# Kernel tuning notes

Measured on AMD Instinct MI355X. Metric: run time of the kernel, lower is better.

The kernel has to match this reference:

```python
import jax, jax.numpy as jnp
import numpy as np

B, E, H = 4096, 8, 1024
XDIM, ZDIM, ODIM, GH = 800, 64, 768, 128

def setup_inputs() -> dict:
    key = jax.random.key(0)
    ks = jax.random.split(key, 16)
    s = lambda k, shape, fan: jax.random.normal(k, shape, jnp.float32) / np.sqrt(fan)
    return {
        'x': jax.random.normal(ks[0], (B, XDIM), jnp.float32),
        'z': jax.random.normal(ks[1], (B, ZDIM), jnp.float32),
        'Wg1': s(ks[2], (GH, XDIM + ZDIM), XDIM + ZDIM),
        'bg1': jnp.zeros((GH,), jnp.float32),
        'Wg2': s(ks[3], (GH, GH), GH),
        'bg2': jnp.zeros((GH,), jnp.float32),
        'Wg3': s(ks[4], (E, GH), GH),
        'bg3': jnp.zeros((E,), jnp.float32),
        'W0': s(ks[5], (E, H, XDIM + ZDIM), XDIM + ZDIM),
        'b0': jnp.zeros((E, H), jnp.float32),
        'W1': s(ks[6], (E, H, H + ZDIM), H + ZDIM),
        'b1': jnp.zeros((E, H), jnp.float32),
        'W2': s(ks[7], (E, H, H + ZDIM), H + ZDIM),
        'b2': jnp.zeros((E, H), jnp.float32),
        'W3': s(ks[8], (E, ODIM, H), H),
        'b3': jnp.zeros((E, ODIM), jnp.float32),
    }

def _blended_layer(bc, inp, W, b):
    # equivalent to (sum_e bc_e W_e) @ inp + sum_e bc_e b_e, but computed as
    # per-expert matmul then weighted accumulation (avoids [B,out,in] blend).
    y = jnp.einsum('bi,eoi->beo', inp, W)          # per-expert outputs
    return jnp.einsum('be,beo->bo', bc, y) + bc @ b

def reference(x, z, Wg1, bg1, Wg2, bg2, Wg3, bg3,
              W0, b0, W1, b1, W2, b2, W3, b3):
    g = jnp.concatenate([x, z], axis=1)
    h = jax.nn.elu(g @ Wg1.T + bg1)
    h = jax.nn.elu(h @ Wg2.T + bg2)
    bc = jax.nn.softmax(h @ Wg3.T + bg3, axis=-1)  # [B, E] blend coefficients
    h = jax.nn.elu(_blended_layer(bc, jnp.concatenate([x, z], 1), W0, b0))
    h = jax.nn.elu(_blended_layer(bc, jnp.concatenate([h, z], 1), W1, b1))
    h = jax.nn.elu(_blended_layer(bc, jnp.concatenate([h, z], 1), W2, b2))
    return _blended_layer(bc, h, W3, b3)  # [B, ODIM], no activation
```

## Files before the change

kernel.cpp:

```cpp
#include <hip/hip_runtime.h>
#include <math.h>

#define BDIM 4096
#define NEXP 8
#define HDIM 1024
#define XDIM 800
#define ZDIM 64
#define ODIM 768
#define GH   128

typedef _Float16 f16;
typedef f16   f16x8 __attribute__((ext_vector_type(8)));
typedef f16   f16x4 __attribute__((ext_vector_type(4)));
typedef float f32x4 __attribute__((ext_vector_type(4)));

__device__ __forceinline__ float elu_act(float x) {
    return x > 0.0f ? x : expm1f(x);
}

__device__ __forceinline__ void glds16(const void* g, void* l) {
    __builtin_amdgcn_global_load_lds(
        (const __attribute__((address_space(1))) void*)g,
        (__attribute__((address_space(3))) void*)l, 16, 0, 0);
}

__device__ __forceinline__ f16x8 vscale(f16x8 v, f16 s) {
    f16x8 r;
    #pragma unroll
    for (int i = 0; i < 8; ++i) r[i] = v[i] * s;
    return r;
}

#define BMg 64
#define BNg 64
#define BKg 32
#define PADg 68

template<int ACT>
__global__ __launch_bounds__(256)
void gemm_cat(const float* __restrict__ srcA, int KH,
              const float* __restrict__ srcZ, int KZ,
              const float* __restrict__ W, const float* __restrict__ bias,
              float* __restrict__ dst, int N)
{
    __shared__ float lds_a[BKg][PADg];
    __shared__ float lds_b[BKg][PADg];
    const int K = KH + KZ;
    const int row0 = blockIdx.x * BMg;
    const int col0 = blockIdx.y * BNg;
    const int tid = threadIdx.x;
    const int tx = tid & 15, ty = tid >> 4;

    float acc[4][4] = {};

    for (int k0 = 0; k0 < K; k0 += BKg) {
        #pragma unroll
        for (int it = 0; it < 2; ++it) {
            int idx = tid + it * 256;
            int r = idx >> 3;
            int f = idx & 7;
            int k = k0 + f * 4;
            const float* src; int col;
            if (k < KH) { src = srcA + (size_t)(row0 + r) * KH; col = k; }
            else        { src = srcZ + (size_t)(row0 + r) * KZ; col = k - KH; }
            float4 v = *(const float4*)(src + col);
            lds_a[f*4+0][r] = v.x; lds_a[f*4+1][r] = v.y;
            lds_a[f*4+2][r] = v.z; lds_a[f*4+3][r] = v.w;
        }
        #pragma unroll
        for (int it = 0; it < 2; ++it) {
            int idx = tid + it * 256;
            int c = idx >> 3;
            int f = idx & 7;
            int k = k0 + f * 4;
            float4 v = *(const float4*)(W + (size_t)(col0 + c) * K + k);
            lds_b[f*4+0][c] = v.x; lds_b[f*4+1][c] = v.y;
            lds_b[f*4+2][c] = v.z; lds_b[f*4+3][c] = v.w;
        }
        __syncthreads();
        #pragma unroll
        for (int j = 0; j < BKg; ++j) {
            float4 a4 = *(const float4*)&lds_a[j][ty*4];
            float4 b4 = *(const float4*)&lds_b[j][tx*4];
            float a[4] = {a4.x, a4.y, a4.z, a4.w};
            float b[4] = {b4.x, b4.y, b4.z, b4.w};
            #pragma unroll
            for (int i = 0; i < 4; ++i)
                #pragma unroll
                for (int jj = 0; jj < 4; ++jj)
                    acc[i][jj] += a[i] * b[jj];
        }
        __syncthreads();
    }

    #pragma unroll
    for (int i = 0; i < 4; ++i) {
        int r = row0 + ty*4 + i;
        float vals[4];
        #pragma unroll
        for (int j = 0; j < 4; ++j) {
            float v = acc[i][j] + bias[col0 + tx*4 + j];
            vals[j] = (ACT == 1) ? elu_act(v) : v;
        }
        *(float4*)(dst + (size_t)r * N + col0 + tx*4) =
            make_float4(vals[0], vals[1], vals[2], vals[3]);
    }
}

__global__ __launch_bounds__(256)
void gating3_softmax(const float* __restrict__ g2, const float* __restrict__ Wg3,
                     const float* __restrict__ bg3, float* __restrict__ bc)
{
    __shared__ float w[NEXP * GH];
    __shared__ float bsh[NEXP];
    const int tid = threadIdx.x;
    for (int i = tid; i < NEXP * GH; i += 256) w[i] = Wg3[i];
    if (tid < NEXP) bsh[tid] = bg3[tid];
    __syncthreads();

    const int rowl = tid >> 3;
    const int o    = tid & 7;
    const int row  = blockIdx.x * 32 + rowl;
    const float* g = g2 + (size_t)row * GH;

    float s = bsh[o];
    for (int k = 0; k < GH; ++k) s += g[k] * w[o * GH + k];

    float m = s;
    #pragma unroll
    for (int d = 4; d >= 1; d >>= 1) m = fmaxf(m, __shfl_xor(m, d, 8));
    float e = expf(s - m);
    float sum = e;
    #pragma unroll
    for (int d = 4; d >= 1; d >>= 1) sum += __shfl_xor(sum, d, 8);

    bc[(size_t)blockIdx.x * 256 + tid] = e / sum;
}

__global__ __launch_bounds__(256)
void fill_z(const float* __restrict__ z, f16* __restrict__ hz_a,
            f16* __restrict__ hz_b)
{
    int i = (blockIdx.x * 256 + threadIdx.x) * 4;
    int row = i >> 6;
    int col = i & 63;
    float4 v = *(const float4*)(z + i);
    f16x4 o = { (f16)v.x, (f16)v.y, (f16)v.z, (f16)v.w };
    size_t off = (size_t)row * (HDIM + ZDIM) + HDIM + col;
    *(f16x4*)(hz_a + off) = o;
    *(f16x4*)(hz_b + off) = o;
}

__global__ __launch_bounds__(256)
void w_to_f16(const float* __restrict__ src, f16* __restrict__ dst)
{
    size_t i = ((size_t)blockIdx.x * 256 + threadIdx.x) * 8;
    float4 v0 = *(const float4*)(src + i);
    float4 v1 = *(const float4*)(src + i + 4);
    f16x8 o = { (f16)v0.x,(f16)v0.y,(f16)v0.z,(f16)v0.w,
                (f16)v1.x,(f16)v1.y,(f16)v1.z,(f16)v1.w };
    *(f16x8*)(dst + i) = o;
}

template<int KE, int N, int ACT, int SRC, typename OT>
__global__ __launch_bounds__(256, 2)
void blended_big(const f16* __restrict__ A, int ldA,
                 const float* __restrict__ x, const float* __restrict__ z,
                 const f16* __restrict__ Wf, const float* __restrict__ bias,
                 const float* __restrict__ bc, OT* __restrict__ out, int ldOut)
{
    constexpr int NCT = N / 128;
    __shared__ __align__(16) f16 a_sh[64][40];
    __shared__ __align__(16) f16 b_sh[NEXP * 128 * 32];
    __shared__ float bc_sh[64][8];
    __shared__ float bias_sh[8][128];

    const int tid  = threadIdx.x;
    const int bid  = blockIdx.x;
    const int row0 = (bid / NCT) * 64;
    const int col0 = (bid % NCT) * 128;
    const int wave = tid >> 6;
    const int lane = tid & 63;
    const int ln   = lane & 15;
    const int quad = lane >> 4;
    const int wy   = wave >> 1;
    const int wx   = wave & 1;

    for (int i = tid; i < 64 * 8; i += 256)
        bc_sh[i >> 3][i & 7] = bc[(size_t)(row0 + (i >> 3)) * NEXP + (i & 7)];
    for (int i = tid; i < 8 * 128; i += 256)
        bias_sh[i >> 7][i & 127] = bias[(size_t)(i >> 7) * N + col0 + (i & 127)];

    f16 bcf[2][8];
    #pragma unroll
    for (int mi = 0; mi < 2; ++mi) {
        const float* bp = bc + (size_t)(row0 + wy*32 + mi*16 + ln) * NEXP;
        #pragma unroll
        for (int e = 0; e < NEXP; ++e) bcf[mi][e] = (f16)bp[e];
    }

    const int ar = tid >> 2;
    const int ac = tid & 3;
    const int kcl  = (lane & 3) ^ ((lane >> 3) & 3);
    const int prow = lane >> 2;
    const f16* wb[2];
    #pragma unroll
    for (int ee = 0; ee < 2; ++ee)
        wb[ee] = Wf + ((size_t)(wave*2 + ee) * N + col0 + prow) * KE + kcl * 8;

    const int csel = quad ^ ((ln >> 1) & 3);

    f32x4 acc[2][4] = {};

    for (int k0 = 0; k0 < KE; k0 += 32) {
        __syncthreads();

        #pragma unroll
        for (int ee = 0; ee < 2; ++ee) {
            const int e = wave * 2 + ee;
            #pragma unroll
            for (int j = 0; j < 8; ++j) {
                glds16(wb[ee] + k0 + (size_t)j * 16 * KE,
                       &b_sh[(e * 128 + j * 16) * 32]);
            }
        }

        f16x8 av;
        if (SRC == 0) {
            int k = k0 + ac * 8;
            const float* s = (k < XDIM)
                ? x + (size_t)(row0 + ar) * XDIM + k
                : z + (size_t)(row0 + ar) * ZDIM + (k - XDIM);
            float4 v0 = *(const float4*)s;
            float4 v1 = *(const float4*)(s + 4);
            av = (f16x8){ (f16)v0.x,(f16)v0.y,(f16)v0.z,(f16)v0.w,
                          (f16)v1.x,(f16)v1.y,(f16)v1.z,(f16)v1.w };
        } else {
            av = *(const f16x8*)(A + (size_t)(row0 + ar) * ldA + k0 + ac * 8);
        }
        *(f16x8*)&a_sh[ar][ac * 8] = av;

        __syncthreads();

        f16x8 af0 = *(const f16x8*)&a_sh[wy*32 +      ln][quad * 8];
        f16x8 af1 = *(const f16x8*)&a_sh[wy*32 + 16 + ln][quad * 8];

        #pragma unroll
        for (int e = 0; e < NEXP; ++e) {
            f16x8 bf[4];
            #pragma unroll
            for (int ni = 0; ni < 4; ++ni) {
                int n = wx*64 + ni*16 + ln;
                bf[ni] = *(const f16x8*)&b_sh[e*4096 + n*32 + csel*8];
            }
            f16x8 a0 = vscale(af0, bcf[0][e]);
            f16x8 a1 = vscale(af1, bcf[1][e]);
            #pragma unroll
            for (int ni = 0; ni < 4; ++ni) {
                acc[0][ni] = __builtin_amdgcn_mfma_f32_16x16x32_f16(
                    a0, bf[ni], acc[0][ni], 0, 0, 0);
                acc[1][ni] = __builtin_amdgcn_mfma_f32_16x16x32_f16(
                    a1, bf[ni], acc[1][ni], 0, 0, 0);
            }
        }
    }

    #pragma unroll
    for (int mi = 0; mi < 2; ++mi)
        #pragma unroll
        for (int r = 0; r < 4; ++r) {
            int rl = wy*32 + mi*16 + quad*4 + r;
            size_t grow = (size_t)(row0 + rl) * ldOut;
            #pragma unroll
            for (int ni = 0; ni < 4; ++ni) {
                int cl = wx*64 + ni*16 + ln;
                float v = acc[mi][ni][r];
                #pragma unroll
                for (int e2 = 0; e2 < NEXP; ++e2)
                    v += bc_sh[rl][e2] * bias_sh[e2][cl];
                if (ACT) v = elu_act(v);
                out[grow + col0 + cl] = (OT)v;
            }
        }
}

extern "C" void kernel_launch(void* const* d_in, const int* in_sizes, int n_in,
                              void* d_out, int out_size, void* d_ws, size_t ws_size,
                              hipStream_t stream)
{
    const float* x   = (const float*)d_in[0];
    const float* z   = (const float*)d_in[1];
    const float* Wg1 = (const float*)d_in[2];
    const float* bg1 = (const float*)d_in[3];
    const float* Wg2 = (const float*)d_in[4];
    const float* bg2 = (const float*)d_in[5];
    const float* Wg3 = (const float*)d_in[6];
    const float* bg3 = (const float*)d_in[7];
    const float* W0  = (const float*)d_in[8];
    const float* b0  = (const float*)d_in[9];
    const float* W1  = (const float*)d_in[10];
    const float* b1  = (const float*)d_in[11];
    const float* W2  = (const float*)d_in[12];
    const float* b2  = (const float*)d_in[13];
    const float* W3  = (const float*)d_in[14];
    const float* b3  = (const float*)d_in[15];
    float* out = (float*)d_out;

    char* ws = (char*)d_ws;
    f16*   wbuf = (f16*)ws;                 ws += (size_t)NEXP * HDIM * (HDIM + ZDIM) * 2;
    f16*   hz_a = (f16*)ws;                 ws += (size_t)BDIM * (HDIM + ZDIM) * 2;
    f16*   hz_b = (f16*)ws;                 ws += (size_t)BDIM * (HDIM + ZDIM) * 2;
    float* g1   = (float*)ws;               ws += (size_t)BDIM * GH * 4;
    float* g2   = (float*)ws;               ws += (size_t)BDIM * GH * 4;
    float* bcw  = (float*)ws;

    dim3 blk(256);

    fill_z<<<dim3(BDIM * ZDIM / 4 / 256), blk, 0, stream>>>(z, hz_a, hz_b);

    gemm_cat<1><<<dim3(BDIM/BMg, GH/BNg), blk, 0, stream>>>(x, XDIM, z, ZDIM, Wg1, bg1, g1, GH);
    gemm_cat<1><<<dim3(BDIM/BMg, GH/BNg), blk, 0, stream>>>(g1, GH, nullptr, 0, Wg2, bg2, g2, GH);
    gating3_softmax<<<dim3(BDIM/32), blk, 0, stream>>>(g2, Wg3, bg3, bcw);

    w_to_f16<<<dim3(NEXP*HDIM*(XDIM+ZDIM)/8/256), blk, 0, stream>>>(W0, wbuf);
    blended_big<XDIM+ZDIM, HDIM, 1, 0, f16><<<dim3(64 * 8), blk, 0, stream>>>(
        nullptr, 0, x, z, wbuf, b0, bcw, hz_a, HDIM + ZDIM);

    w_to_f16<<<dim3(NEXP*HDIM*(HDIM+ZDIM)/8/256), blk, 0, stream>>>(W1, wbuf);
    blended_big<HDIM+ZDIM, HDIM, 1, 1, f16><<<dim3(64 * 8), blk, 0, stream>>>(
        hz_a, HDIM + ZDIM, nullptr, nullptr, wbuf, b1, bcw, hz_b, HDIM + ZDIM);

    w_to_f16<<<dim3(NEXP*HDIM*(HDIM+ZDIM)/8/256), blk, 0, stream>>>(W2, wbuf);
    blended_big<HDIM+ZDIM, HDIM, 1, 1, f16><<<dim3(64 * 8), blk, 0, stream>>>(
        hz_b, HDIM + ZDIM, nullptr, nullptr, wbuf, b2, bcw, hz_a, HDIM + ZDIM);

    w_to_f16<<<dim3(NEXP*ODIM*HDIM/8/256), blk, 0, stream>>>(W3, wbuf);
    blended_big<HDIM, ODIM, 0, 1, float><<<dim3(64 * 6), blk, 0, stream>>>(
        hz_a, HDIM + ZDIM, nullptr, nullptr, wbuf, b3, bcw, out, ODIM);
}
```

Measured before the change: 620.1 us.

## Pre-tile expert weights into MFMA fragment order and load B directly to registers

The weight conversion kernel now writes f16 weights in a tiled layout that matches the MFMA B-fragment order, so the blended GEMM kernel can read B operands straight from global memory into registers and no longer stages them through LDS with global_load_lds. Block output tiles shrink from 64x128 to 64x64, which doubles the grid, and the occupancy hint rises to 4 blocks per CU. The A tile is double-buffered and the next A slice and next expert's B fragments are prefetched in software. The aim is to remove the large LDS staging and its barriers. In exchange, B-tile reuse across waves in a block is lost, so global and L2 traffic for weights rises.

```diff
diff --git a/kernel.cpp b/kernel.cpp
--- a/kernel.cpp
+++ b/kernel.cpp
@@ -16,12 +16,6 @@
 
 __device__ __forceinline__ float elu_act(float x) {
     return x > 0.0f ? x : expm1f(x);
-}
-
-__device__ __forceinline__ void glds16(const void* g, void* l) {
-    __builtin_amdgcn_global_load_lds(
-        (const __attribute__((address_space(1))) void*)g,
-        (__attribute__((address_space(3))) void*)l, 16, 0, 0);
 }
 
 __device__ __forceinline__ f16x8 vscale(f16x8 v, f16 s) {
@@ -151,34 +145,43 @@
     *(f16x4*)(hz_b + off) = o;
 }
 
+template<int N, int K>
 __global__ __launch_bounds__(256)
-void w_to_f16(const float* __restrict__ src, f16* __restrict__ dst)
-{
-    size_t i = ((size_t)blockIdx.x * 256 + threadIdx.x) * 8;
-    float4 v0 = *(const float4*)(src + i);
-    float4 v1 = *(const float4*)(src + i + 4);
+void w_tile(const float* __restrict__ W, f16* __restrict__ Wt)
+{
+    constexpr int KC = K / 32;
+    size_t i = (size_t)blockIdx.x * 256 + threadIdx.x;
+    int lane = (int)(i & 63);
+    size_t t = i >> 6;
+    int kc = (int)(t % KC);
+    int nt = (int)((t / KC) % (N / 16));
+    int e  = (int)(t / KC / (N / 16));
+    const float* s = W + ((size_t)e * N + nt * 16 + (lane & 15)) * K
+                       + kc * 32 + (lane >> 4) * 8;
+    float4 v0 = *(const float4*)s;
+    float4 v1 = *(const float4*)(s + 4);
     f16x8 o = { (f16)v0.x,(f16)v0.y,(f16)v0.z,(f16)v0.w,
                 (f16)v1.x,(f16)v1.y,(f16)v1.z,(f16)v1.w };
-    *(f16x8*)(dst + i) = o;
-}
-
-template<int KE, int N, int ACT, int SRC, typename OT>
-__global__ __launch_bounds__(256, 2)
-void blended_big(const f16* __restrict__ A, int ldA,
-                 const float* __restrict__ x, const float* __restrict__ z,
-                 const f16* __restrict__ Wf, const float* __restrict__ bias,
-                 const float* __restrict__ bc, OT* __restrict__ out, int ldOut)
-{
-    constexpr int NCT = N / 128;
-    __shared__ __align__(16) f16 a_sh[64][40];
-    __shared__ __align__(16) f16 b_sh[NEXP * 128 * 32];
+    *(f16x8*)(Wt + i * 8) = o;
+}
+
+template<int K, int N, int ACT, int SRC, typename OT>
+__global__ __launch_bounds__(256, 4)
+void blended_v2(const f16* __restrict__ A, int ldA,
+                const float* __restrict__ x, const float* __restrict__ z,
+                const f16* __restrict__ Wt, const float* __restrict__ bias,
+                const float* __restrict__ bc, OT* __restrict__ out, int ldOut)
+{
+    constexpr int KC  = K / 32;
+    constexpr int NCT = N / 64;
+    __shared__ __align__(16) f16 a_sh[2][64][40];
     __shared__ float bc_sh[64][8];
-    __shared__ float bias_sh[8][128];
+    __shared__ float bias_sh[8][64];
 
     const int tid  = threadIdx.x;
     const int bid  = blockIdx.x;
     const int row0 = (bid / NCT) * 64;
-    const int col0 = (bid % NCT) * 128;
+    const int col0 = (bid % NCT) * 64;
     const int wave = tid >> 6;
     const int lane = tid & 63;
     const int ln   = lane & 15;
@@ -188,93 +191,84 @@
 
     for (int i = tid; i < 64 * 8; i += 256)
         bc_sh[i >> 3][i & 7] = bc[(size_t)(row0 + (i >> 3)) * NEXP + (i & 7)];
-    for (int i = tid; i < 8 * 128; i += 256)
-        bias_sh[i >> 7][i & 127] = bias[(size_t)(i >> 7) * N + col0 + (i & 127)];
-
-    f16 bcf[2][8];
-    #pragma unroll
-    for (int mi = 0; mi < 2; ++mi) {
-        const float* bp = bc + (size_t)(row0 + wy*32 + mi*16 + ln) * NEXP;
-        #pragma unroll
-        for (int e = 0; e < NEXP; ++e) bcf[mi][e] = (f16)bp[e];
-    }
+    for (int i = tid; i < 8 * 64; i += 256)
+        bias_sh[i >> 6][i & 63] = bias[(size_t)(i >> 6) * N + col0 + (i & 63)];
 
     const int ar = tid >> 2;
     const int ac = tid & 3;
-    const int kcl  = (lane & 3) ^ ((lane >> 3) & 3);
-    const int prow = lane >> 2;
-    const f16* wb[2];
-    #pragma unroll
-    for (int ee = 0; ee < 2; ++ee)
-        wb[ee] = Wf + ((size_t)(wave*2 + ee) * N + col0 + prow) * KE + kcl * 8;
-
-    const int csel = quad ^ ((ln >> 1) & 3);
-
-    f32x4 acc[2][4] = {};
-
-    for (int k0 = 0; k0 < KE; k0 += 32) {
-        __syncthreads();
-
-        #pragma unroll
-        for (int ee = 0; ee < 2; ++ee) {
-            const int e = wave * 2 + ee;
-            #pragma unroll
-            for (int j = 0; j < 8; ++j) {
-                glds16(wb[ee] + k0 + (size_t)j * 16 * KE,
-                       &b_sh[(e * 128 + j * 16) * 32]);
-            }
-        }
-
-        f16x8 av;
+
+    auto loadA = [&](int ks) -> f16x8 {
+        int k = ks * 32 + ac * 8;
         if (SRC == 0) {
-            int k = k0 + ac * 8;
             const float* s = (k < XDIM)
                 ? x + (size_t)(row0 + ar) * XDIM + k
                 : z + (size_t)(row0 + ar) * ZDIM + (k - XDIM);
             float4 v0 = *(const float4*)s;
             float4 v1 = *(const float4*)(s + 4);
-            av = (f16x8){ (f16)v0.x,(f16)v0.y,(f16)v0.z,(f16)v0.w,
-                          (f16)v1.x,(f16)v1.y,(f16)v1.z,(f16)v1.w };
+            return (f16x8){ (f16)v0.x,(f16)v0.y,(f16)v0.z,(f16)v0.w,
+                            (f16)v1.x,(f16)v1.y,(f16)v1.z,(f16)v1.w };
         } else {
-            av = *(const f16x8*)(A + (size_t)(row0 + ar) * ldA + k0 + ac * 8);
-        }
-        *(f16x8*)&a_sh[ar][ac * 8] = av;
-
+            return *(const f16x8*)(A + (size_t)(row0 + ar) * ldA + k);
+        }
+    };
+
+    f16x8 av = loadA(0);
+
+    __syncthreads();
+
+    f16 bcf[2][8];
+    #pragma unroll
+    for (int mt = 0; mt < 2; ++mt)
+        #pragma unroll
+        for (int e = 0; e < 8; ++e)
+            bcf[mt][e] = (f16)bc_sh[wy*32 + mt*16 + ln][e];
+
+    const f16* wp = Wt + ((size_t)(col0/16 + wx*2) * KC) * 512 + lane * 8;
+    constexpr size_t ESTR = (size_t)(N/16) * KC * 512;
+    constexpr size_t TSTR = (size_t)KC * 512;
+
+    f32x4 acc[2][2] = {};
+
+    for (int ks = 0; ks < KC; ++ks) {
+        *(f16x8*)&a_sh[ks & 1][ar][ac * 8] = av;
         __syncthreads();
 
-        f16x8 af0 = *(const f16x8*)&a_sh[wy*32 +      ln][quad * 8];
-        f16x8 af1 = *(const f16x8*)&a_sh[wy*32 + 16 + ln][quad * 8];
-
-        #pragma unroll
-        for (int e = 0; e < NEXP; ++e) {
-            f16x8 bf[4];
-            #pragma unroll
-            for (int ni = 0; ni < 4; ++ni) {
-                int n = wx*64 + ni*16 + ln;
-                bf[ni] = *(const f16x8*)&b_sh[e*4096 + n*32 + csel*8];
+        if (ks + 1 < KC) av = loadA(ks + 1);
+
+        f16x8 af0 = *(const f16x8*)&a_sh[ks & 1][wy*32 +      ln][quad * 8];
+        f16x8 af1 = *(const f16x8*)&a_sh[ks & 1][wy*32 + 16 + ln][quad * 8];
+
+        const f16* wk = wp + (size_t)ks * 512;
+        f16x8 b0 = *(const f16x8*)(wk);
+        f16x8 b1 = *(const f16x8*)(wk + TSTR);
+
+        #pragma unroll
+        for (int e = 0; e < 8; ++e) {
+            f16x8 nb0 = b0, nb1 = b1;
+            if (e < 7) {
+                nb0 = *(const f16x8*)(wk + (size_t)(e+1) * ESTR);
+                nb1 = *(const f16x8*)(wk + (size_t)(e+1) * ESTR + TSTR);
             }
-            f16x8 a0 = vscale(af0, bcf[0][e]);
-            f16x8 a1 = vscale(af1, bcf[1][e]);
-            #pragma unroll
-            for (int ni = 0; ni < 4; ++ni) {
-                acc[0][ni] = __builtin_amdgcn_mfma_f32_16x16x32_f16(
-                    a0, bf[ni], acc[0][ni], 0, 0, 0);
-                acc[1][ni] = __builtin_amdgcn_mfma_f32_16x16x32_f16(
-                    a1, bf[ni], acc[1][ni], 0, 0, 0);
-            }
+            f16x8 s0 = vscale(af0, bcf[0][e]);
+            f16x8 s1 = vscale(af1, bcf[1][e]);
+            acc[0][0] = __builtin_amdgcn_mfma_f32_16x16x32_f16(s0, b0, acc[0][0], 0,0,0);
+            acc[0][1] = __builtin_amdgcn_mfma_f32_16x16x32_f16(s0, b1, acc[0][1], 0,0,0);
+            acc[1][0] = __builtin_amdgcn_mfma_f32_16x16x32_f16(s1, b0, acc[1][0], 0,0,0);
+            acc[1][1] = __builtin_amdgcn_mfma_f32_16x16x32_f16(s1, b1, acc[1][1], 0,0,0);
+            b0 = nb0; b1 = nb1;
         }
     }
 
     #pragma unroll
-    for (int mi = 0; mi < 2; ++mi)
+    for (int mt = 0; mt < 2; ++mt)
         #pragma unroll
         for (int r = 0; r < 4; ++r) {
-            int rl = wy*32 + mi*16 + quad*4 + r;
+            int rl = wy*32 + mt*16 + quad*4 + r;
             size_t grow = (size_t)(row0 + rl) * ldOut;
             #pragma unroll
-            for (int ni = 0; ni < 4; ++ni) {
-                int cl = wx*64 + ni*16 + ln;
-                float v = acc[mi][ni][r];
+            for (int nt = 0; nt < 2; ++nt) {
+                int cl = wx*32 + nt*16 + ln;
+                float v = acc[mt][nt][r];
                 #pragma unroll
                 for (int e2 = 0; e2 < NEXP; ++e2)
                     v += bc_sh[rl][e2] * bias_sh[e2][cl];
@@ -322,19 +316,19 @@
     gemm_cat<1><<<dim3(BDIM/BMg, GH/BNg), blk, 0, stream>>>(g1, GH, nullptr, 0, Wg2, bg2, g2, GH);
     gating3_softmax<<<dim3(BDIM/32), blk, 0, stream>>>(g2, Wg3, bg3, bcw);
 
-    w_to_f16<<<dim3(NEXP*HDIM*(XDIM+ZDIM)/8/256), blk, 0, stream>>>(W0, wbuf);
-    blended_big<XDIM+ZDIM, HDIM, 1, 0, f16><<<dim3(64 * 8), blk, 0, stream>>>(
+    w_tile<HDIM, XDIM+ZDIM><<<dim3(NEXP*HDIM*(XDIM+ZDIM)/8/256), blk, 0, stream>>>(W0, wbuf);
+    blended_v2<XDIM+ZDIM, HDIM, 1, 0, f16><<<dim3(64 * 16), blk, 0, stream>>>(
         nullptr, 0, x, z, wbuf, b0, bcw, hz_a, HDIM + ZDIM);
 
-    w_to_f16<<<dim3(NEXP*HDIM*(HDIM+ZDIM)/8/256), blk, 0, stream>>>(W1, wbuf);
-    blended_big<HDIM+ZDIM, HDIM, 1, 1, f16><<<dim3(64 * 8), blk, 0, stream>>>(
+    w_tile<HDIM, HDIM+ZDIM><<<dim3(NEXP*HDIM*(HDIM+ZDIM)/8/256), blk, 0, stream>>>(W1, wbuf);
+    blended_v2<HDIM+ZDIM, HDIM, 1, 1, f16><<<dim3(64 * 16), blk, 0, stream>>>(
         hz_a, HDIM + ZDIM, nullptr, nullptr, wbuf, b1, bcw, hz_b, HDIM + ZDIM);
 
-    w_to_f16<<<dim3(NEXP*HDIM*(HDIM+ZDIM)/8/256), blk, 0, stream>>>(W2, wbuf);
-    blended_big<HDIM+ZDIM, HDIM, 1, 1, f16><<<dim3(64 * 8), blk, 0, stream>>>(
+    w_tile<HDIM, HDIM+ZDIM><<<dim3(NEXP*HDIM*(HDIM+ZDIM)/8/256), blk, 0, stream>>>(W2, wbuf);
+    blended_v2<HDIM+ZDIM, HDIM, 1, 1, f16><<<dim3(64 * 16), blk, 0, stream>>>(
         hz_b, HDIM + ZDIM, nullptr, nullptr, wbuf, b2, bcw, hz_a, HDIM + ZDIM);
 
-    w_to_f16<<<dim3(NEXP*ODIM*HDIM/8/256), blk, 0, stream>>>(W3, wbuf);
-    blended_big<HDIM, ODIM, 0, 1, float><<<dim3(64 * 6), blk, 0, stream>>>(
+    w_tile<ODIM, HDIM><<<dim3(NEXP*ODIM*HDIM/8/256), blk, 0, stream>>>(W3, wbuf);
+    blended_v2<HDIM, ODIM, 0, 1, float><<<dim3(64 * 12), blk, 0, stream>>>(
         hz_a, HDIM + ZDIM, nullptr, nullptr, wbuf, b3, bcw, out, ODIM);
 }
```

Measured after the change: 650.1 us. +4.8%, slower.
